# Kernel optimization log

Hardware: AMD Instinct MI355X
Metric: run time of the kernel (lower is better)

The kernel has to match this reference:

```python
import jax, jax.numpy as jnp
import numpy as np

N_BINS = 32
RANGE_MIN, RANGE_MAX = -3.0, 3.0
MIN_BIN = 1e-5
MIN_SLOPE = 1e-5


def _norm_sizes(u):
    # distrax _normalize_bin_sizes: softmax, rescale so sizes sum to range, floor at MIN_BIN
    total = RANGE_MAX - RANGE_MIN
    return jax.nn.softmax(u, axis=-1) * (total - N_BINS * MIN_BIN) + MIN_BIN


def _norm_slopes(u):
    # distrax _normalize_knot_slopes: softplus with offset so u=0 -> slope 1
    offset = np.float32(np.log(np.exp(1.0 - MIN_SLOPE) - 1.0))
    return jax.nn.softplus(u + offset) + MIN_SLOPE


def rqs_forward(x, params):
    # x: [B], params: [B, 3*N_BINS+1]; monotone rational-quadratic spline forward
    w = _norm_sizes(params[:, :N_BINS])              # [B, N_BINS] bin widths
    h = _norm_sizes(params[:, N_BINS:2 * N_BINS])    # [B, N_BINS] bin heights
    d = _norm_slopes(params[:, 2 * N_BINS:])         # [B, N_BINS+1] knot slopes
    xpos = RANGE_MIN + jnp.pad(jnp.cumsum(w, axis=-1), ((0, 0), (1, 0)))  # [B, N_BINS+1]
    ypos = RANGE_MIN + jnp.pad(jnp.cumsum(h, axis=-1), ((0, 0), (1, 0)))
    # per-element bin search over the N_BINS+1 knots
    idx = jnp.clip(jnp.sum((x[:, None] >= xpos).astype(jnp.int32), axis=-1) - 1, 0, N_BINS - 1)

    def g(a):
        return jnp.take_along_axis(a, idx[:, None], axis=-1)[:, 0]

    xk, wk = g(xpos[:, :-1]), g(w)
    yk, hk = g(ypos[:, :-1]), g(h)
    dk, dk1 = g(d[:, :-1]), g(d[:, 1:])
    z = jnp.clip((x - xk) / wk, 0.0, 1.0)
    s = hk / wk
    z1 = z * (1.0 - z)
    num = hk * (s * z * z + dk * z1)
    den = s + (dk1 + dk - 2.0 * s) * z1
    y = yk + num / den
    # identity outside [RANGE_MIN, RANGE_MAX]
    return jnp.where((x < RANGE_MIN) | (x > RANGE_MAX), x, y)


def setup_inputs() -> dict:
    key = jax.random.key(0)
    ks = jax.random.split(key, 12)
    B, D, H = 262144, 64, 256
    P = 3 * N_BINS + 1
    L = 4
    inp = {
        "cond": jax.random.normal(ks[0], (B, D), jnp.float32),
        "t": jax.random.normal(ks[1], (B, 1), jnp.float32),
        "w1": jax.random.normal(ks[2], (D, H), jnp.float32) / np.sqrt(D),
        "b1": jnp.zeros((H,), jnp.float32),
        "w2": jax.random.normal(ks[3], (H, H), jnp.float32) / np.sqrt(H),
        "b2": jnp.zeros((H,), jnp.float32),
        "spline_w": jax.random.normal(ks[4], (L, H, P), jnp.float32) / np.sqrt(H),
        "spline_b": jnp.zeros((L, P), jnp.float32),
        "aff_w": jax.random.normal(ks[5], (H, 4), jnp.float32) / np.sqrt(H),
        "aff_b": jnp.zeros((4,), jnp.float32),
    }
    return inp


def reference(cond, t, w1, b1, w2, b2, spline_w, spline_b, aff_w, aff_b):
    latent = jax.nn.relu(cond @ w1 + b1)
    latent = jax.nn.relu(latent @ w2 + b2)          # [B, 256]
    sa = latent @ aff_w + aff_b                      # [B, 4]
    # f_1: scale * t + shift (ScalarAffine with log_scale)
    x = (t * jnp.exp(sa[:, 1:2]) + sa[:, 0:1])[:, 0]
    # distrax.Chain applies the LAST bijector in the list first
    for i in range(spline_w.shape[0] - 1, -1, -1):
        p = latent @ spline_w[i] + spline_b[i]       # [B, 3*N_BINS+1]
        x = rqs_forward(x, p)
    # f_2
    x = x[:, None] * jnp.exp(sa[:, 3:4]) + sa[:, 2:3]
    return jax.scipy.stats.norm.cdf(x)
```

## Files before the change

### kernel.cpp

```cpp
#include <hip/hip_runtime.h>
#include <math.h>

#define NB 32

typedef _Float16 half_t;
typedef _Float16 half8 __attribute__((ext_vector_type(8)));
typedef float f32x4 __attribute__((ext_vector_type(4)));

#define FR_G1  0
#define FR_G2  32
#define FR_SP  160
#define FR_AFF 384
#define FR_TOTAL 392

__device__ __forceinline__ void split16(float x, half_t& h, half_t& l) {
    h = (half_t)x;
    l = (half_t)(x - (float)h);
}

__global__ __launch_bounds__(64) void prep_kernel(
    const float* __restrict__ w1, const float* __restrict__ w2,
    const float* __restrict__ sw, const float* __restrict__ aw,
    half_t* __restrict__ frags)
{
    const int f = blockIdx.x;
    const int l = threadIdx.x;
    const int kl = (l >> 4) * 8;
    const int nl = l & 15;
    half8 vh, vl;
    #pragma unroll
    for (int j = 0; j < 8; ++j) {
        float w = 0.f;
        if (f < FR_G2) {
            int ks = f >> 4, ct = f & 15;
            w = w1[(ks * 32 + kl + j) * 256 + ct * 16 + nl];
        } else if (f < FR_SP) {
            int g = f - FR_G2;
            int ks = g >> 4, ct = g & 15;
            w = w2[(ks * 32 + kl + j) * 256 + ct * 16 + nl];
        } else if (f < FR_AFF) {
            int g = f - FR_SP;
            int layer = g / 56, r = g - layer * 56;
            int ks = r / 7, ct = r - ks * 7;
            int n = ct * 16 + nl;
            if (n < 97) w = sw[(size_t)layer * 24832 + (size_t)(ks * 32 + kl + j) * 97 + n];
        } else {
            int ks = f - FR_AFF;
            if (nl < 4) w = aw[(ks * 32 + kl + j) * 4 + nl];
        }
        half_t h, lo;
        split16(w, h, lo);
        vh[j] = h; vl[j] = lo;
    }
    *reinterpret_cast<half8*>(frags + (size_t)f * 512 + l * 8) = vh;
    *reinterpret_cast<half8*>(frags + (size_t)(FR_TOTAL + f) * 512 + l * 8) = vl;
}

__device__ __forceinline__ float softplus_f(float v) {
    return v > 0.f ? v + log1pf(__expf(-v)) : log1pf(__expf(v));
}

__device__ __forceinline__ float rqs_coop2(float x, const float* __restrict__ p, int lane) {
    const float RMIN = -3.0f;
    const float total = 6.0f - 32.0f * 1e-5f;
    const float OFF = 0.54130903f;
    const int l2 = lane & 1;
    const int b0 = l2 * 16;

    float mw = -INFINITY, mh = -INFINITY;
    #pragma unroll
    for (int i = 0; i < 16; ++i) {
        mw = fmaxf(mw, p[b0 + i]);
        mh = fmaxf(mh, p[NB + b0 + i]);
    }
    mw = fmaxf(mw, __shfl_xor(mw, 1));
    mh = fmaxf(mh, __shfl_xor(mh, 1));

    float swd = 0.f, shd = 0.f;
    #pragma unroll
    for (int i = 0; i < 16; ++i) {
        swd += __expf(p[b0 + i] - mw);
        shd += __expf(p[NB + b0 + i] - mh);
    }
    float swdo = __shfl_xor(swd, 1);
    float shdo = __shfl_xor(shd, 1);
    float sw_scale = total / (swd + swdo);
    float sh_scale = total / (shd + shdo);
    float prew = l2 ? (swdo * sw_scale + 16.f * 1e-5f) : 0.f;
    float preh = l2 ? (shdo * sh_scale + 16.f * 1e-5f) : 0.f;

    float cumw = 0.f, cumh = 0.f;
    float cw_c = 0.f, ch_c = 0.f, wk_c = 1.f, hk_c = 1.f;
    int idx_c = 0, cap = 0;
    #pragma unroll
    for (int i = 0; i < 16; ++i) {
        float wi = __expf(p[b0 + i] - mw) * sw_scale + 1e-5f;
        float hi = __expf(p[NB + b0 + i] - mh) * sh_scale + 1e-5f;
        float lw = prew + cumw;
        if (x >= RMIN + lw) {
            cw_c = lw; ch_c = preh + cumh; wk_c = wi; hk_c = hi;
            idx_c = b0 + i; cap = 1;
        }
        cumw += wi; cumh += hi;
    }

    const int hi_l = lane | 1, lo_l = lane & ~1;
    int   cap1 = __shfl(cap,  hi_l);
    float cw1 = __shfl(cw_c, hi_l), cw0 = __shfl(cw_c, lo_l);
    float ch1 = __shfl(ch_c, hi_l), ch0 = __shfl(ch_c, lo_l);
    float wk1 = __shfl(wk_c, hi_l), wk0 = __shfl(wk_c, lo_l);
    float hk1 = __shfl(hk_c, hi_l), hk0 = __shfl(hk_c, lo_l);
    int   ix1 = __shfl(idx_c, hi_l), ix0 = __shfl(idx_c, lo_l);
    float cw = cap1 ? cw1 : cw0;
    float ch = cap1 ? ch1 : ch0;
    float wk = cap1 ? wk1 : wk0;
    float hk = cap1 ? hk1 : hk0;
    int   idx = cap1 ? ix1 : ix0;

    float dk  = softplus_f(p[2 * NB + idx] + OFF) + 1e-5f;
    float dk1 = softplus_f(p[2 * NB + idx + 1] + OFF) + 1e-5f;

    float xk = RMIN + cw, yk = RMIN + ch;
    float z = (x - xk) / wk;
    z = fminf(fmaxf(z, 0.f), 1.f);
    float s = hk / wk;
    float z1 = z * (1.f - z);
    float num = hk * (s * z * z + dk * z1);
    float den = s + (dk1 + dk - 2.f * s) * z1;
    float y = yk + num / den;
    return (x < -3.0f || x > 3.0f) ? x : y;
}

#define LT 264
#define PST 105

__global__ __launch_bounds__(512, 4) void condflow_kernel(
    const float* __restrict__ cond, const float* __restrict__ t_in,
    const float* __restrict__ b1, const float* __restrict__ b2,
    const float* __restrict__ sb, const float* __restrict__ ab,
    const half_t* __restrict__ frags,
    float* __restrict__ out)
{
    __shared__ half_t lat16h[32 * LT];
    __shared__ half_t lat16l[32 * LT];
    __shared__ float pbuf[32][PST];
    __shared__ float sa_s[32][4];

    const int t    = threadIdx.x;
    const int row0 = blockIdx.x * 32;
    const int wid  = t >> 6;
    const int lane = t & 63;
    const int q    = lane >> 4;
    const int nl   = lane & 15;
    const half_t* fr_lo = frags + (size_t)FR_TOTAL * 512;

    {
        f32x4 c[2][2];
        #pragma unroll
        for (int rt = 0; rt < 2; ++rt)
            #pragma unroll
            for (int ic = 0; ic < 2; ++ic) c[rt][ic] = f32x4{0.f, 0.f, 0.f, 0.f};

        #pragma unroll
        for (int ks = 0; ks < 2; ++ks) {
            half8 ah[2], al[2];
            #pragma unroll
            for (int rt = 0; rt < 2; ++rt) {
                const float* src = cond + (size_t)(row0 + rt * 16 + nl) * 64 + ks * 32 + q * 8;
                float4 v0 = *reinterpret_cast<const float4*>(src);
                float4 v1 = *reinterpret_cast<const float4*>(src + 4);
                float vv[8] = {v0.x, v0.y, v0.z, v0.w, v1.x, v1.y, v1.z, v1.w};
                #pragma unroll
                for (int j = 0; j < 8; ++j) { half_t h, l; split16(vv[j], h, l); ah[rt][j] = h; al[rt][j] = l; }
            }
            #pragma unroll
            for (int ic = 0; ic < 2; ++ic) {
                int fidx = FR_G1 + ks * 16 + (wid * 2 + ic);
                half8 bh = *reinterpret_cast<const half8*>(frags + (size_t)fidx * 512 + lane * 8);
                half8 bl = *reinterpret_cast<const half8*>(fr_lo + (size_t)fidx * 512 + lane * 8);
                #pragma unroll
                for (int rt = 0; rt < 2; ++rt) {
                    c[rt][ic] = __builtin_amdgcn_mfma_f32_16x16x32_f16(ah[rt], bh, c[rt][ic], 0, 0, 0);
                    c[rt][ic] = __builtin_amdgcn_mfma_f32_16x16x32_f16(al[rt], bh, c[rt][ic], 0, 0, 0);
                    c[rt][ic] = __builtin_amdgcn_mfma_f32_16x16x32_f16(ah[rt], bl, c[rt][ic], 0, 0, 0);
                }
            }
        }
        #pragma unroll
        for (int ic = 0; ic < 2; ++ic) {
            int col = (wid * 2 + ic) * 16 + nl;
            float bv = b1[col];
            #pragma unroll
            for (int rt = 0; rt < 2; ++rt)
                #pragma unroll
                for (int reg = 0; reg < 4; ++reg) {
                    float y = fmaxf(c[rt][ic][reg] + bv, 0.f);
                    half_t h, l; split16(y, h, l);
                    int off = (rt * 16 + q * 4 + reg) * LT + col;
                    lat16h[off] = h; lat16l[off] = l;
                }
        }
    }
    __syncthreads();

    {
        f32x4 c[2][2];
        #pragma unroll
        for (int rt = 0; rt < 2; ++rt)
            #pragma unroll
            for (int ic = 0; ic < 2; ++ic) c[rt][ic] = f32x4{0.f, 0.f, 0.f, 0.f};

        #pragma unroll
        for (int ks = 0; ks < 8; ++ks) {
            half8 ah[2], al[2];
            #pragma unroll
            for (int rt = 0; rt < 2; ++rt) {
                int off = (rt * 16 + nl) * LT + ks * 32 + q * 8;
                ah[rt] = *reinterpret_cast<const half8*>(lat16h + off);
                al[rt] = *reinterpret_cast<const half8*>(lat16l + off);
            }
            #pragma unroll
            for (int ic = 0; ic < 2; ++ic) {
                int fidx = FR_G2 + ks * 16 + (wid * 2 + ic);
                half8 bh = *reinterpret_cast<const half8*>(frags + (size_t)fidx * 512 + lane * 8);
                half8 bl = *reinterpret_cast<const half8*>(fr_lo + (size_t)fidx * 512 + lane * 8);
                #pragma unroll
                for (int rt = 0; rt < 2; ++rt) {
                    c[rt][ic] = __builtin_amdgcn_mfma_f32_16x16x32_f16(ah[rt], bh, c[rt][ic], 0, 0, 0);
                    c[rt][ic] = __builtin_amdgcn_mfma_f32_16x16x32_f16(al[rt], bh, c[rt][ic], 0, 0, 0);
                    c[rt][ic] = __builtin_amdgcn_mfma_f32_16x16x32_f16(ah[rt], bl, c[rt][ic], 0, 0, 0);
                }
            }
        }
        __syncthreads();
        #pragma unroll
        for (int ic = 0; ic < 2; ++ic) {
            int col = (wid * 2 + ic) * 16 + nl;
            float bv = b2[col];
            #pragma unroll
            for (int rt = 0; rt < 2; ++rt)
                #pragma unroll
                for (int reg = 0; reg < 4; ++reg) {
                    float y = fmaxf(c[rt][ic][reg] + bv, 0.f);
                    half_t h, l; split16(y, h, l);
                    int off = (rt * 16 + q * 4 + reg) * LT + col;
                    lat16h[off] = h; lat16l[off] = l;
                }
        }
    }
    __syncthreads();

    float x = 0.f;

    for (int layer = 3; layer >= 0; --layer) {
        f32x4 cp[2];
        cp[0] = f32x4{0.f, 0.f, 0.f, 0.f};
        cp[1] = f32x4{0.f, 0.f, 0.f, 0.f};

        if (wid >= 1) {
            const int ct = wid - 1;
            #pragma unroll
            for (int ks = 0; ks < 8; ++ks) {
                half8 ah[2], al[2];
                #pragma unroll
                for (int rt = 0; rt < 2; ++rt) {
                    int off = (rt * 16 + nl) * LT + ks * 32 + q * 8;
                    ah[rt] = *reinterpret_cast<const half8*>(lat16h + off);
                    al[rt] = *reinterpret_cast<const half8*>(lat16l + off);
                }
                int fidx = FR_SP + layer * 56 + ks * 7 + ct;
                half8 bh = *reinterpret_cast<const half8*>(frags + (size_t)fidx * 512 + lane * 8);
                #pragma unroll
                for (int rt = 0; rt < 2; ++rt) {
                    cp[rt] = __builtin_amdgcn_mfma_f32_16x16x32_f16(ah[rt], bh, cp[rt], 0, 0, 0);
                    cp[rt] = __builtin_amdgcn_mfma_f32_16x16x32_f16(al[rt], bh, cp[rt], 0, 0, 0);
                }
            }
        } else if (layer == 3) {
            #pragma unroll
            for (int ks = 0; ks < 8; ++ks) {
                half8 bh = *reinterpret_cast<const half8*>(frags + (size_t)(FR_AFF + ks) * 512 + lane * 8);
                half8 bl = *reinterpret_cast<const half8*>(fr_lo + (size_t)(FR_AFF + ks) * 512 + lane * 8);
                #pragma unroll
                for (int rt = 0; rt < 2; ++rt) {
                    int off = (rt * 16 + nl) * LT + ks * 32 + q * 8;
                    half8 ah = *reinterpret_cast<const half8*>(lat16h + off);
                    half8 al = *reinterpret_cast<const half8*>(lat16l + off);
                    cp[rt] = __builtin_amdgcn_mfma_f32_16x16x32_f16(ah, bh, cp[rt], 0, 0, 0);
                    cp[rt] = __builtin_amdgcn_mfma_f32_16x16x32_f16(al, bh, cp[rt], 0, 0, 0);
                    cp[rt] = __builtin_amdgcn_mfma_f32_16x16x32_f16(ah, bl, cp[rt], 0, 0, 0);
                }
            }
            if (nl < 4) {
                float abv = ab[nl];
                #pragma unroll
                for (int rt = 0; rt < 2; ++rt)
                    #pragma unroll
                    for (int reg = 0; reg < 4; ++reg)
                        sa_s[rt * 16 + q * 4 + reg][nl] = cp[rt][reg] + abv;
            }
        }

        __syncthreads();
        if (wid >= 1) {
            int n0 = (wid - 1) * 16 + nl;
            if (n0 < 97) {
                float sbv = sb[layer * 97 + n0];
                #pragma unroll
                for (int rt = 0; rt < 2; ++rt)
                    #pragma unroll
                    for (int reg = 0; reg < 4; ++reg)
                        pbuf[rt * 16 + q * 4 + reg][n0] = cp[rt][reg] + sbv;
            }
        }
        __syncthreads();
        if (t < 64) {
            int rrow = t >> 1;
            if (layer == 3) x = t_in[row0 + rrow] * __expf(sa_s[rrow][1]) + sa_s[rrow][0];
            x = rqs_coop2(x, &pbuf[rrow][0], t);
            if (layer == 0 && (t & 1) == 0) {
                float xf = x * __expf(sa_s[rrow][3]) + sa_s[rrow][2];
                out[row0 + rrow] = 0.5f * (1.0f + erff(xf * 0.70710678118f));
            }
        }
    }
}

extern "C" void kernel_launch(void* const* d_in, const int* in_sizes, int n_in,
                              void* d_out, int out_size, void* d_ws, size_t ws_size,
                              hipStream_t stream) {
    const float* cond = (const float*)d_in[0];
    const float* t_in = (const float*)d_in[1];
    const float* w1   = (const float*)d_in[2];
    const float* b1   = (const float*)d_in[3];
    const float* w2   = (const float*)d_in[4];
    const float* b2   = (const float*)d_in[5];
    const float* sw   = (const float*)d_in[6];
    const float* sb   = (const float*)d_in[7];
    const float* aw   = (const float*)d_in[8];
    const float* ab   = (const float*)d_in[9];
    float* out = (float*)d_out;

    half_t* frags = (half_t*)d_ws;

    prep_kernel<<<dim3(FR_TOTAL), dim3(64), 0, stream>>>(w1, w2, sw, aw, frags);

    const int B = out_size;
    const int nblocks = B / 32;
    condflow_kernel<<<dim3(nblocks), dim3(512), 0, stream>>>(
        cond, t_in, b1, b2, sb, ab, frags, out);
}
```

Before: 388.4 us.

## Compute two spline layers' parameter GEMMs per pass to share latent loads

The four-layer spline loop becomes two passes. Each pass computes the parameter matmuls for two layers at once, reusing the same latent A-fragments loaded from shared memory, and writes both parameter sets into a widened pbuf. Two RQS evaluations then run back to back. This halves the number of barrier pairs and the LDS reads of the latent. In exchange, pbuf roughly doubles in size, which may cut the number of blocks resident per CU, and accumulator register use grows.

```diff
diff --git a/kernel.cpp b/kernel.cpp
--- a/kernel.cpp
+++ b/kernel.cpp
@@ -132,7 +132,7 @@
 }
 
 #define LT 264
-#define PST 105
+#define PST 209
 
 __global__ __launch_bounds__(512, 4) void condflow_kernel(
     const float* __restrict__ cond, const float* __restrict__ t_in,
@@ -252,10 +252,14 @@
 
     float x = 0.f;
 
-    for (int layer = 3; layer >= 0; --layer) {
-        f32x4 cp[2];
-        cp[0] = f32x4{0.f, 0.f, 0.f, 0.f};
-        cp[1] = f32x4{0.f, 0.f, 0.f, 0.f};
+    #pragma unroll
+    for (int pass = 0; pass < 2; ++pass) {
+        const int Lhi = 3 - 2 * pass;
+        f32x4 cp[2][2];
+        #pragma unroll
+        for (int L = 0; L < 2; ++L)
+            #pragma unroll
+            for (int rt = 0; rt < 2; ++rt) cp[L][rt] = f32x4{0.f, 0.f, 0.f, 0.f};
 
         if (wid >= 1) {
             const int ct = wid - 1;
@@ -268,15 +272,18 @@
                     ah[rt] = *reinterpret_cast<const half8*>(lat16h + off);
                     al[rt] = *reinterpret_cast<const half8*>(lat16l + off);
                 }
-                int fidx = FR_SP + layer * 56 + ks * 7 + ct;
-                half8 bh = *reinterpret_cast<const half8*>(frags + (size_t)fidx * 512 + lane * 8);
-                #pragma unroll
-                for (int rt = 0; rt < 2; ++rt) {
-                    cp[rt] = __builtin_amdgcn_mfma_f32_16x16x32_f16(ah[rt], bh, cp[rt], 0, 0, 0);
-                    cp[rt] = __builtin_amdgcn_mfma_f32_16x16x32_f16(al[rt], bh, cp[rt], 0, 0, 0);
-                }
-            }
-        } else if (layer == 3) {
+                #pragma unroll
+                for (int L = 0; L < 2; ++L) {
+                    int fidx = FR_SP + (Lhi - L) * 56 + ks * 7 + ct;
+                    half8 bh = *reinterpret_cast<const half8*>(frags + (size_t)fidx * 512 + lane * 8);
+                    #pragma unroll
+                    for (int rt = 0; rt < 2; ++rt) {
+                        cp[L][rt] = __builtin_amdgcn_mfma_f32_16x16x32_f16(ah[rt], bh, cp[L][rt], 0, 0, 0);
+                        cp[L][rt] = __builtin_amdgcn_mfma_f32_16x16x32_f16(al[rt], bh, cp[L][rt], 0, 0, 0);
+                    }
+                }
+            }
+        } else if (pass == 0) {
             #pragma unroll
             for (int ks = 0; ks < 8; ++ks) {
                 half8 bh = *reinterpret_cast<const half8*>(frags + (size_t)(FR_AFF + ks) * 512 + lane * 8);
@@ -286,9 +293,9 @@
                     int off = (rt * 16 + nl) * LT + ks * 32 + q * 8;
                     half8 ah = *reinterpret_cast<const half8*>(lat16h + off);
                     half8 al = *reinterpret_cast<const half8*>(lat16l + off);
-                    cp[rt] = __builtin_amdgcn_mfma_f32_16x16x32_f16(ah, bh, cp[rt], 0, 0, 0);
-                    cp[rt] = __builtin_amdgcn_mfma_f32_16x16x32_f16(al, bh, cp[rt], 0, 0, 0);
-                    cp[rt] = __builtin_amdgcn_mfma_f32_16x16x32_f16(ah, bl, cp[rt], 0, 0, 0);
+                    cp[0][rt] = __builtin_amdgcn_mfma_f32_16x16x32_f16(ah, bh, cp[0][rt], 0, 0, 0);
+                    cp[0][rt] = __builtin_amdgcn_mfma_f32_16x16x32_f16(al, bh, cp[0][rt], 0, 0, 0);
+                    cp[0][rt] = __builtin_amdgcn_mfma_f32_16x16x32_f16(ah, bl, cp[0][rt], 0, 0, 0);
                 }
             }
             if (nl < 4) {
@@ -297,7 +304,7 @@
                 for (int rt = 0; rt < 2; ++rt)
                     #pragma unroll
                     for (int reg = 0; reg < 4; ++reg)
-                        sa_s[rt * 16 + q * 4 + reg][nl] = cp[rt][reg] + abv;
+                        sa_s[rt * 16 + q * 4 + reg][nl] = cp[0][rt][reg] + abv;
             }
         }
 
@@ -305,20 +312,25 @@
         if (wid >= 1) {
             int n0 = (wid - 1) * 16 + nl;
             if (n0 < 97) {
-                float sbv = sb[layer * 97 + n0];
+                float sbh = sb[Lhi * 97 + n0];
+                float sbl = sb[(Lhi - 1) * 97 + n0];
                 #pragma unroll
                 for (int rt = 0; rt < 2; ++rt)
                     #pragma unroll
-                    for (int reg = 0; reg < 4; ++reg)
-                        pbuf[rt * 16 + q * 4 + reg][n0] = cp[rt][reg] + sbv;
+                    for (int reg = 0; reg < 4; ++reg) {
+                        int r = rt * 16 + q * 4 + reg;
+                        pbuf[r][n0]       = cp[0][rt][reg] + sbh;
+                        pbuf[r][104 + n0] = cp[1][rt][reg] + sbl;
+                    }
             }
         }
         __syncthreads();
         if (t < 64) {
             int rrow = t >> 1;
-            if (layer == 3) x = t_in[row0 + rrow] * __expf(sa_s[rrow][1]) + sa_s[rrow][0];
+            if (pass == 0) x = t_in[row0 + rrow] * __expf(sa_s[rrow][1]) + sa_s[rrow][0];
             x = rqs_coop2(x, &pbuf[rrow][0], t);
-            if (layer == 0 && (t & 1) == 0) {
+            x = rqs_coop2(x, &pbuf[rrow][104], t);
+            if (pass == 1 && (t & 1) == 0) {
                 float xf = x * __expf(sa_s[rrow][3]) + sa_s[rrow][2];
                 out[row0 + rrow] = 0.5f * (1.0f + erff(xf * 0.70710678118f));
             }
```

Result: slower. 397.4 us (+2.3%).

## Double rows per block and compute two spline layers per pass

Applied to the files above, without the earlier changes.

Each block now handles 64 rows with 1024 threads. Every wave computes one 16-column strip across four row tiles, so each weight fragment load is reused over more rows. The spline-parameter GEMMs for two layers are computed together in one pass, with 14 waves covering both layers' 7 column tiles. This halves the number of syncs and serial spline phases, and the two splines are then applied back to back by 128 threads. The cost is much larger LDS use per block (about 121 KB), which may cut occupancy, and a longer serial spline section per pass.

```diff
diff --git a/kernel.cpp b/kernel.cpp
--- a/kernel.cpp
+++ b/kernel.cpp
@@ -132,22 +132,22 @@
 }
 
 #define LT 264
-#define PST 105
-
-__global__ __launch_bounds__(512, 4) void condflow_kernel(
+#define PST 209
+
+__global__ __launch_bounds__(1024, 4) void condflow_kernel(
     const float* __restrict__ cond, const float* __restrict__ t_in,
     const float* __restrict__ b1, const float* __restrict__ b2,
     const float* __restrict__ sb, const float* __restrict__ ab,
     const half_t* __restrict__ frags,
     float* __restrict__ out)
 {
-    __shared__ half_t lat16h[32 * LT];
-    __shared__ half_t lat16l[32 * LT];
-    __shared__ float pbuf[32][PST];
-    __shared__ float sa_s[32][4];
+    __shared__ half_t lat16h[64 * LT];
+    __shared__ half_t lat16l[64 * LT];
+    __shared__ float pbuf[64][PST];
+    __shared__ float sa_s[64][4];
 
     const int t    = threadIdx.x;
-    const int row0 = blockIdx.x * 32;
+    const int row0 = blockIdx.x * 64;
     const int wid  = t >> 6;
     const int lane = t & 63;
     const int q    = lane >> 4;
@@ -155,17 +155,15 @@
     const half_t* fr_lo = frags + (size_t)FR_TOTAL * 512;
 
     {
-        f32x4 c[2][2];
-        #pragma unroll
-        for (int rt = 0; rt < 2; ++rt)
-            #pragma unroll
-            for (int ic = 0; ic < 2; ++ic) c[rt][ic] = f32x4{0.f, 0.f, 0.f, 0.f};
+        f32x4 c[4];
+        #pragma unroll
+        for (int rt = 0; rt < 4; ++rt) c[rt] = f32x4{0.f, 0.f, 0.f, 0.f};
 
         #pragma unroll
         for (int ks = 0; ks < 2; ++ks) {
-            half8 ah[2], al[2];
-            #pragma unroll
-            for (int rt = 0; rt < 2; ++rt) {
+            half8 ah[4], al[4];
+            #pragma unroll
+            for (int rt = 0; rt < 4; ++rt) {
                 const float* src = cond + (size_t)(row0 + rt * 16 + nl) * 64 + ks * 32 + q * 8;
                 float4 v0 = *reinterpret_cast<const float4*>(src);
                 float4 v1 = *reinterpret_cast<const float4*>(src + 4);
@@ -173,97 +171,87 @@
                 #pragma unroll
                 for (int j = 0; j < 8; ++j) { half_t h, l; split16(vv[j], h, l); ah[rt][j] = h; al[rt][j] = l; }
             }
-            #pragma unroll
-            for (int ic = 0; ic < 2; ++ic) {
-                int fidx = FR_G1 + ks * 16 + (wid * 2 + ic);
-                half8 bh = *reinterpret_cast<const half8*>(frags + (size_t)fidx * 512 + lane * 8);
-                half8 bl = *reinterpret_cast<const half8*>(fr_lo + (size_t)fidx * 512 + lane * 8);
-                #pragma unroll
-                for (int rt = 0; rt < 2; ++rt) {
-                    c[rt][ic] = __builtin_amdgcn_mfma_f32_16x16x32_f16(ah[rt], bh, c[rt][ic], 0, 0, 0);
-                    c[rt][ic] = __builtin_amdgcn_mfma_f32_16x16x32_f16(al[rt], bh, c[rt][ic], 0, 0, 0);
-                    c[rt][ic] = __builtin_amdgcn_mfma_f32_16x16x32_f16(ah[rt], bl, c[rt][ic], 0, 0, 0);
-                }
-            }
-        }
-        #pragma unroll
-        for (int ic = 0; ic < 2; ++ic) {
-            int col = (wid * 2 + ic) * 16 + nl;
-            float bv = b1[col];
-            #pragma unroll
-            for (int rt = 0; rt < 2; ++rt)
-                #pragma unroll
-                for (int reg = 0; reg < 4; ++reg) {
-                    float y = fmaxf(c[rt][ic][reg] + bv, 0.f);
-                    half_t h, l; split16(y, h, l);
-                    int off = (rt * 16 + q * 4 + reg) * LT + col;
-                    lat16h[off] = h; lat16l[off] = l;
-                }
-        }
+            int fidx = FR_G1 + ks * 16 + wid;
+            half8 bh = *reinterpret_cast<const half8*>(frags + (size_t)fidx * 512 + lane * 8);
+            half8 bl = *reinterpret_cast<const half8*>(fr_lo + (size_t)fidx * 512 + lane * 8);
+            #pragma unroll
+            for (int rt = 0; rt < 4; ++rt) {
+                c[rt] = __builtin_amdgcn_mfma_f32_16x16x32_f16(ah[rt], bh, c[rt], 0, 0, 0);
+                c[rt] = __builtin_amdgcn_mfma_f32_16x16x32_f16(al[rt], bh, c[rt], 0, 0, 0);
+                c[rt] = __builtin_amdgcn_mfma_f32_16x16x32_f16(ah[rt], bl, c[rt], 0, 0, 0);
+            }
+        }
+        int col = wid * 16 + nl;
+        float bv = b1[col];
+        #pragma unroll
+        for (int rt = 0; rt < 4; ++rt)
+            #pragma unroll
+            for (int reg = 0; reg < 4; ++reg) {
+                float y = fmaxf(c[rt][reg] + bv, 0.f);
+                half_t h, l; split16(y, h, l);
+                int off = (rt * 16 + q * 4 + reg) * LT + col;
+                lat16h[off] = h; lat16l[off] = l;
+            }
     }
     __syncthreads();
 
     {
-        f32x4 c[2][2];
-        #pragma unroll
-        for (int rt = 0; rt < 2; ++rt)
-            #pragma unroll
-            for (int ic = 0; ic < 2; ++ic) c[rt][ic] = f32x4{0.f, 0.f, 0.f, 0.f};
+        f32x4 c[4];
+        #pragma unroll
+        for (int rt = 0; rt < 4; ++rt) c[rt] = f32x4{0.f, 0.f, 0.f, 0.f};
 
         #pragma unroll
         for (int ks = 0; ks < 8; ++ks) {
-            half8 ah[2], al[2];
-            #pragma unroll
-            for (int rt = 0; rt < 2; ++rt) {
+            half8 ah[4], al[4];
+            #pragma unroll
+            for (int rt = 0; rt < 4; ++rt) {
                 int off = (rt * 16 + nl) * LT + ks * 32 + q * 8;
                 ah[rt] = *reinterpret_cast<const half8*>(lat16h + off);
                 al[rt] = *reinterpret_cast<const half8*>(lat16l + off);
             }
-            #pragma unroll
-            for (int ic = 0; ic < 2; ++ic) {
-                int fidx = FR_G2 + ks * 16 + (wid * 2 + ic);
-                half8 bh = *reinterpret_cast<const half8*>(frags + (size_t)fidx * 512 + lane * 8);
-                half8 bl = *reinterpret_cast<const half8*>(fr_lo + (size_t)fidx * 512 + lane * 8);
-                #pragma unroll
-                for (int rt = 0; rt < 2; ++rt) {
-                    c[rt][ic] = __builtin_amdgcn_mfma_f32_16x16x32_f16(ah[rt], bh, c[rt][ic], 0, 0, 0);
-                    c[rt][ic] = __builtin_amdgcn_mfma_f32_16x16x32_f16(al[rt], bh, c[rt][ic], 0, 0, 0);
-                    c[rt][ic] = __builtin_amdgcn_mfma_f32_16x16x32_f16(ah[rt], bl, c[rt][ic], 0, 0, 0);
-                }
+            int fidx = FR_G2 + ks * 16 + wid;
+            half8 bh = *reinterpret_cast<const half8*>(frags + (size_t)fidx * 512 + lane * 8);
+            half8 bl = *reinterpret_cast<const half8*>(fr_lo + (size_t)fidx * 512 + lane * 8);
+            #pragma unroll
+            for (int rt = 0; rt < 4; ++rt) {
+                c[rt] = __builtin_amdgcn_mfma_f32_16x16x32_f16(ah[rt], bh, c[rt], 0, 0, 0);
+                c[rt] = __builtin_amdgcn_mfma_f32_16x16x32_f16(al[rt], bh, c[rt], 0, 0, 0);
+                c[rt] = __builtin_amdgcn_mfma_f32_16x16x32_f16(ah[rt], bl, c[rt], 0, 0, 0);
             }
         }
         __syncthreads();
-        #pragma unroll
-        for (int ic = 0; ic < 2; ++ic) {
-            int col = (wid * 2 + ic) * 16 + nl;
-            float bv = b2[col];
-            #pragma unroll
-            for (int rt = 0; rt < 2; ++rt)
-                #pragma unroll
-                for (int reg = 0; reg < 4; ++reg) {
-                    float y = fmaxf(c[rt][ic][reg] + bv, 0.f);
-                    half_t h, l; split16(y, h, l);
-                    int off = (rt * 16 + q * 4 + reg) * LT + col;
-                    lat16h[off] = h; lat16l[off] = l;
-                }
-        }
+        int col = wid * 16 + nl;
+        float bv = b2[col];
+        #pragma unroll
+        for (int rt = 0; rt < 4; ++rt)
+            #pragma unroll
+            for (int reg = 0; reg < 4; ++reg) {
+                float y = fmaxf(c[rt][reg] + bv, 0.f);
+                half_t h, l; split16(y, h, l);
+                int off = (rt * 16 + q * 4 + reg) * LT + col;
+                lat16h[off] = h; lat16l[off] = l;
+            }
     }
     __syncthreads();
 
     float x = 0.f;
 
-    for (int layer = 3; layer >= 0; --layer) {
-        f32x4 cp[2];
-        cp[0] = f32x4{0.f, 0.f, 0.f, 0.f};
-        cp[1] = f32x4{0.f, 0.f, 0.f, 0.f};
-
-        if (wid >= 1) {
-            const int ct = wid - 1;
+    #pragma unroll
+    for (int pass = 0; pass < 2; ++pass) {
+        const int Lhi = 3 - 2 * pass;
+        f32x4 cp[4];
+        #pragma unroll
+        for (int rt = 0; rt < 4; ++rt) cp[rt] = f32x4{0.f, 0.f, 0.f, 0.f};
+
+        if (wid >= 2) {
+            const int sidx = wid - 2;
+            const int ct = sidx >> 1;
+            const int layer = Lhi - (sidx & 1);
             #pragma unroll
             for (int ks = 0; ks < 8; ++ks) {
-                half8 ah[2], al[2];
-                #pragma unroll
-                for (int rt = 0; rt < 2; ++rt) {
+                half8 ah[4], al[4];
+                #pragma unroll
+                for (int rt = 0; rt < 4; ++rt) {
                     int off = (rt * 16 + nl) * LT + ks * 32 + q * 8;
                     ah[rt] = *reinterpret_cast<const half8*>(lat16h + off);
                     al[rt] = *reinterpret_cast<const half8*>(lat16l + off);
@@ -271,18 +259,18 @@
                 int fidx = FR_SP + layer * 56 + ks * 7 + ct;
                 half8 bh = *reinterpret_cast<const half8*>(frags + (size_t)fidx * 512 + lane * 8);
                 #pragma unroll
-                for (int rt = 0; rt < 2; ++rt) {
+                for (int rt = 0; rt < 4; ++rt) {
                     cp[rt] = __builtin_amdgcn_mfma_f32_16x16x32_f16(ah[rt], bh, cp[rt], 0, 0, 0);
                     cp[rt] = __builtin_amdgcn_mfma_f32_16x16x32_f16(al[rt], bh, cp[rt], 0, 0, 0);
                 }
             }
-        } else if (layer == 3) {
+        } else if (pass == 0 && wid == 0) {
             #pragma unroll
             for (int ks = 0; ks < 8; ++ks) {
                 half8 bh = *reinterpret_cast<const half8*>(frags + (size_t)(FR_AFF + ks) * 512 + lane * 8);
                 half8 bl = *reinterpret_cast<const half8*>(fr_lo + (size_t)(FR_AFF + ks) * 512 + lane * 8);
                 #pragma unroll
-                for (int rt = 0; rt < 2; ++rt) {
+                for (int rt = 0; rt < 4; ++rt) {
                     int off = (rt * 16 + nl) * LT + ks * 32 + q * 8;
                     half8 ah = *reinterpret_cast<const half8*>(lat16h + off);
                     half8 al = *reinterpret_cast<const half8*>(lat16l + off);
@@ -294,7 +282,7 @@
             if (nl < 4) {
                 float abv = ab[nl];
                 #pragma unroll
-                for (int rt = 0; rt < 2; ++rt)
+                for (int rt = 0; rt < 4; ++rt)
                     #pragma unroll
                     for (int reg = 0; reg < 4; ++reg)
                         sa_s[rt * 16 + q * 4 + reg][nl] = cp[rt][reg] + abv;
@@ -302,23 +290,29 @@
         }
 
         __syncthreads();
-        if (wid >= 1) {
-            int n0 = (wid - 1) * 16 + nl;
+        if (wid >= 2) {
+            const int sidx = wid - 2;
+            const int ct = sidx >> 1;
+            const int L = sidx & 1;
+            int n0 = ct * 16 + nl;
             if (n0 < 97) {
-                float sbv = sb[layer * 97 + n0];
-                #pragma unroll
-                for (int rt = 0; rt < 2; ++rt)
+                float sbv = sb[(Lhi - L) * 97 + n0];
+                int base = L ? 104 + n0 : n0;
+                #pragma unroll
+                for (int rt = 0; rt < 4; ++rt)
                     #pragma unroll
                     for (int reg = 0; reg < 4; ++reg)
-                        pbuf[rt * 16 + q * 4 + reg][n0] = cp[rt][reg] + sbv;
+                        pbuf[rt * 16 + q * 4 + reg][base] = cp[rt][reg] + sbv;
             }
         }
         __syncthreads();
-        if (t < 64) {
+        if (t < 128) {
             int rrow = t >> 1;
-            if (layer == 3) x = t_in[row0 + rrow] * __expf(sa_s[rrow][1]) + sa_s[rrow][0];
-            x = rqs_coop2(x, &pbuf[rrow][0], t);
-            if (layer == 0 && (t & 1) == 0) {
+            int rl = t & 63;
+            if (pass == 0) x = t_in[row0 + rrow] * __expf(sa_s[rrow][1]) + sa_s[rrow][0];
+            x = rqs_coop2(x, &pbuf[rrow][0], rl);
+            x = rqs_coop2(x, &pbuf[rrow][104], rl);
+            if (pass == 1 && (t & 1) == 0) {
                 float xf = x * __expf(sa_s[rrow][3]) + sa_s[rrow][2];
                 out[row0 + rrow] = 0.5f * (1.0f + erff(xf * 0.70710678118f));
             }
@@ -346,7 +340,7 @@
     prep_kernel<<<dim3(FR_TOTAL), dim3(64), 0, stream>>>(w1, w2, sw, aw, frags);
 
     const int B = out_size;
-    const int nblocks = B / 32;
-    condflow_kernel<<<dim3(nblocks), dim3(512), 0, stream>>>(
+    const int nblocks = B / 64;
+    condflow_kernel<<<dim3(nblocks), dim3(1024), 0, stream>>>(
         cond, t_in, b1, b2, sb, ab, frags, out);
 }
```

After: 475.4 us. 22.4% more time.
